# Optimization experiments

Hardware: AMD Instinct MI355X
Metric: run time of the kernel (lower is better)

The kernel has to match this reference:

```python
import jax, jax.numpy as jnp
import numpy as np

T, B, IN_DIM, MEM_DIM = 256, 64, 512, 512


def _kaiming(key, shape):
    # kaiming_normal_ default: fan_in = shape[1], gain = sqrt(2)
    std = np.sqrt(2.0 / shape[1])
    return jax.random.normal(key, shape, dtype=jnp.float32) * std


def setup_inputs() -> dict:
    key = jax.random.key(0)
    ks = jax.random.split(key, 10)
    inp = {
        "inputs": jax.random.normal(ks[0], (T, B, IN_DIM), dtype=jnp.float32),
        "emb_s": jax.random.normal(ks[1], (T, B, IN_DIM), dtype=jnp.float32),
        "c0": jnp.zeros((B, MEM_DIM), dtype=jnp.float32),
        "h0": jnp.zeros((B, MEM_DIM), dtype=jnp.float32),
        # learned params (torch Linear: y = x @ W.T + b)
        "W_ioux": _kaiming(ks[2], (4 * MEM_DIM, IN_DIM)),
        "b_ioux": jnp.zeros((4 * MEM_DIM,), jnp.float32),
        "W_iouh": _kaiming(ks[3], (4 * MEM_DIM, MEM_DIM)),
        "b_iouh": jnp.zeros((4 * MEM_DIM,), jnp.float32),
        "W_ious": _kaiming(ks[4], (4 * MEM_DIM, IN_DIM)),
        "b_ious": jnp.zeros((4 * MEM_DIM,), jnp.float32),
        "W_fx": _kaiming(ks[5], (MEM_DIM, IN_DIM)),
        "b_fx": jnp.zeros((MEM_DIM,), jnp.float32),
        "W_fh": _kaiming(ks[6], (MEM_DIM, MEM_DIM)),
        "b_fh": jnp.zeros((MEM_DIM,), jnp.float32),
        "W_wc": _kaiming(ks[7], (MEM_DIM, IN_DIM)),
        "b_wc": jnp.zeros((MEM_DIM,), jnp.float32),
    }
    return inp


def reference(inputs, emb_s, c0, h0,
              W_ioux, b_ioux, W_iouh, b_iouh, W_ious, b_ious,
              W_fx, b_fx, W_fh, b_fh, W_wc, b_wc):
    M = W_fh.shape[0]
    # Precompute all input-dependent projections for the whole sequence (big GEMMs).
    iou_x = (jnp.einsum('tbi,gi->tbg', inputs, W_ioux) + b_ioux
             + jnp.einsum('tbi,gi->tbg', emb_s, W_ious) + b_ious)      # [T,B,4M]
    ctelta_x = jnp.einsum('tbi,mi->tbm', inputs, W_fx) + b_fx          # [T,B,M]
    wc_s = jnp.tanh(jnp.einsum('tbi,mi->tbm', emb_s, W_wc) + b_wc)    # [T,B,M]

    def step(carry, xs):
        c, h = carry
        iou_t, ctx_t, wcs_t = xs
        iou = iou_t + h @ W_iouh.T + b_iouh                            # [B,4M]
        f, i, o, o_c = jnp.split(jax.nn.sigmoid(iou), 4, axis=1)
        c_telta = jnp.tanh(ctx_t + h @ W_fh.T + b_fh)
        c_new = i * c_telta + f * c
        h_new = o * jnp.tanh(c_new) + o_c * wcs_t
        return (c_new, h_new), h_new

    (c_fin, h_fin), out = jax.lax.scan(step, (c0, h0), (iou_x, ctelta_x, wc_s))
    return out, (c_fin, h_fin)
```

## Files before the change

kernel.cpp:

```cpp
#include <hip/hip_runtime.h>
#include <stdint.h>

#define T_STEPS 256
#define B_DIM   64
#define MDIM    512
#define NROWS   (T_STEPS * B_DIM)
#define KCAT    1024
#define NBIG    3072
#define W2ROWS  2560
#define NBLK2   32
#define OUT_N   ((size_t)T_STEPS * B_DIM * MDIM)

typedef short v8s __attribute__((ext_vector_type(8)));
typedef float v4f __attribute__((ext_vector_type(4)));

static __device__ __forceinline__ unsigned short f2bf(float f) {
    unsigned u = __builtin_bit_cast(unsigned, f);
    u += 0x7FFFu + ((u >> 16) & 1u);
    return (unsigned short)(u >> 16);
}
static __device__ __forceinline__ float bf2f(unsigned short h) {
    unsigned u = ((unsigned)h) << 16;
    return __builtin_bit_cast(float, u);
}
static __device__ __forceinline__ float sigmoidf(float x) {
    return 1.0f / (1.0f + __expf(-x));
}


__global__ void pack_xcat(const float* __restrict__ x, const float* __restrict__ s,
                          unsigned short* __restrict__ xcat) {
    int idx = blockIdx.x * blockDim.x + threadIdx.x;
    if (idx >= NROWS * KCAT) return;
    int row = idx >> 10, col = idx & 1023;
    float v = (col < 512) ? x[row * 512 + col] : s[row * 512 + (col - 512)];
    xcat[idx] = f2bf(v);
}

__global__ void pack_wbig(const float* __restrict__ Wioux, const float* __restrict__ bioux,
                          const float* __restrict__ Wious, const float* __restrict__ bious,
                          const float* __restrict__ Wfx,   const float* __restrict__ bfx,
                          const float* __restrict__ Wwc,   const float* __restrict__ bwc,
                          unsigned short* __restrict__ wbig, float* __restrict__ bbig) {
    int idx = blockIdx.x * blockDim.x + threadIdx.x;
    if (idx >= NBIG * KCAT) return;
    int r = idx >> 10, c = idx & 1023;
    float v;
    if (r < 2048)      v = (c < 512) ? Wioux[r * 512 + c] : Wious[r * 512 + (c - 512)];
    else if (r < 2560) { int j = r - 2048; v = (c < 512) ? Wfx[j * 512 + c] : 0.0f; }
    else               { int j = r - 2560; v = (c < 512) ? 0.0f : Wwc[j * 512 + (c - 512)]; }
    wbig[idx] = f2bf(v);
    if (c == 0) {
        float b;
        if (r < 2048)      b = bioux[r] + bious[r];
        else if (r < 2560) b = bfx[r - 2048];
        else               b = bwc[r - 2560];
        bbig[r] = b;
    }
}

__global__ void pack_w2(const float* __restrict__ Wiouh, const float* __restrict__ biouh,
                        const float* __restrict__ Wfh,   const float* __restrict__ bfh,
                        unsigned short* __restrict__ w2, float* __restrict__ b2) {
    int idx = blockIdx.x * blockDim.x + threadIdx.x;
    if (idx >= W2ROWS * 512) return;
    int r = idx >> 9, k = idx & 511;
    int bk = r / 80, rem = r % 80, g = rem >> 4, j = rem & 15;
    int m = bk * 16 + j;
    float v, bias;
    if (g < 4) { v = Wiouh[(size_t)(g * 512 + m) * 512 + k]; bias = biouh[g * 512 + m]; }
    else       { v = Wfh[(size_t)m * 512 + k];               bias = bfh[m]; }
    w2[idx] = f2bf(v);
    if (k == 0) b2[r] = bias;
}

__global__ void init_state(const float* __restrict__ h0,
                           unsigned short* __restrict__ hbuf0,
                           int* __restrict__ cnt) {
    int idx = blockIdx.x * blockDim.x + threadIdx.x;
    if (idx >= B_DIM * MDIM) return;
    hbuf0[idx] = f2bf(h0[idx]);
    if (idx == 0) *cnt = 0;
}


__global__ __launch_bounds__(256) void gemm_big(
        const unsigned short* __restrict__ xcat,
        const unsigned short* __restrict__ wbig,
        const float* __restrict__ bbig,
        unsigned short* __restrict__ yall) {
    __shared__ __align__(16) unsigned short As[128][40];
    __shared__ __align__(16) unsigned short Bs[128][40];
    int nb = blockIdx.x;
    int mb = blockIdx.y;
    int tid = threadIdx.x;
    int lane = tid & 63, wid = tid >> 6;
    int wm = wid & 1, wn = wid >> 1;
    int lm = lane & 15, lq = lane >> 4;
    v4f acc[4][4] = {};
    for (int kb = 0; kb < KCAT / 32; ++kb) {
        __syncthreads();
        #pragma unroll
        for (int it = 0; it < 2; ++it) {
            int cid = tid + it * 256;
            int r = cid >> 2, q = cid & 3;
            *(uint4*)&As[r][q * 8] =
                *(const uint4*)(xcat + (size_t)(mb * 128 + r) * KCAT + kb * 32 + q * 8);
            *(uint4*)&Bs[r][q * 8] =
                *(const uint4*)(wbig + (size_t)(nb * 128 + r) * KCAT + kb * 32 + q * 8);
        }
        __syncthreads();
        v8s a[4], b[4];
        #pragma unroll
        for (int i = 0; i < 4; ++i) a[i] = *(const v8s*)&As[wm * 64 + i * 16 + lm][lq * 8];
        #pragma unroll
        for (int j = 0; j < 4; ++j) b[j] = *(const v8s*)&Bs[wn * 64 + j * 16 + lm][lq * 8];
        #pragma unroll
        for (int i = 0; i < 4; ++i)
            #pragma unroll
            for (int j = 0; j < 4; ++j)
                acc[i][j] = __builtin_amdgcn_mfma_f32_16x16x32_bf16(a[i], b[j], acc[i][j], 0, 0, 0);
    }
    #pragma unroll
    for (int i = 0; i < 4; ++i) {
        int gm = mb * 128 + wm * 64 + i * 16 + lq * 4;
        #pragma unroll
        for (int j = 0; j < 4; ++j) {
            int gn = nb * 128 + wn * 64 + j * 16 + lm;
            float bias = bbig[gn];
            bool do_tanh = (gn >= 2560);
            #pragma unroll
            for (int r = 0; r < 4; ++r) {
                float v = acc[i][j][r] + bias;
                if (do_tanh) v = tanhf(v);
                yall[(size_t)(gm + r) * NBIG + gn] = f2bf(v);
            }
        }
    }
}


__device__ __forceinline__ void grid_barrier(int* cnt, int target) {
    __syncthreads();
    if (threadIdx.x == 0) {
        __hip_atomic_fetch_add(cnt, 1, __ATOMIC_ACQ_REL, __HIP_MEMORY_SCOPE_AGENT);
        while (__hip_atomic_load(cnt, __ATOMIC_ACQUIRE, __HIP_MEMORY_SCOPE_AGENT) < target)
            __builtin_amdgcn_s_sleep(1);
    }
    __syncthreads();
}

__global__ __launch_bounds__(256, 1) void lstm_persist(
        const unsigned short* __restrict__ yall,
        const unsigned short* __restrict__ w2,
        const float* __restrict__ b2,
        const float* __restrict__ c0,
        unsigned short* __restrict__ hbuf0,
        unsigned short* __restrict__ hbuf1,
        float* __restrict__ out,
        int* __restrict__ cnt) {
    __shared__ __align__(16) float red[2][10][256];
    __shared__ __align__(16) unsigned short ybuf[2][64][6][16];
    int bk = blockIdx.x;
    int tid = threadIdx.x;
    int lane = tid & 63, wid = tid >> 6;
    int p = wid >> 1;
    int q = wid & 1;
    int lm = lane & 15, lq = lane >> 4;
    int m = bk * 16 + lm;

    v8s bfrag[5][8];
    const unsigned short* w2b = w2 + (size_t)(bk * 80 + lm) * 512 + lq * 8;
    #pragma unroll
    for (int g = 0; g < 5; ++g)
        #pragma unroll
        for (int j = 0; j < 8; ++j)
            bfrag[g][j] = *(const v8s*)(w2b + (size_t)g * 16 * 512 + (q * 8 + j) * 32);

    float bias[5];
    #pragma unroll
    for (int g = 0; g < 5; ++g) bias[g] = b2[(bk * 5 + g) * 16 + lm];
    float creg[2][4];
    #pragma unroll
    for (int tb = 0; tb < 2; ++tb)
        #pragma unroll
        for (int r = 0; r < 4; ++r)
            creg[tb][r] = c0[(p * 32 + tb * 16 + lq * 4 + r) * 512 + m];

    if (q == 1) {
        #pragma unroll
        for (int i = 0; i < 6; ++i) {
            int c = (p * 6 + i) * 64 + lane;
            int b = c / 12, rem = c % 12, g = rem >> 1, half = rem & 1;
            int gcol = (g < 4) ? g * 512 : (g == 4 ? 2048 : 2560);
            const unsigned short* gp = yall + (size_t)b * NBIG + gcol + bk * 16 + half * 8;
            unsigned short* lp = &ybuf[0][0][0][0] + (p * 6 + i) * 512;
            __builtin_amdgcn_global_load_lds(
                (const __attribute__((address_space(1))) unsigned int*)gp,
                (__attribute__((address_space(3))) unsigned int*)lp, 16, 0, 0);
        }
    }

    for (int t = 0; t < T_STEPS; ++t) {
        const unsigned short* hin = (t & 1) ? hbuf1 : hbuf0;
        unsigned short*      hout = (t & 1) ? hbuf0 : hbuf1;
        v4f acc[2][5] = {};
        const unsigned short* ha = hin + (size_t)(p * 32 + lm) * 512 + q * 256 + lq * 8;
        #pragma unroll
        for (int j = 0; j < 8; ++j) {
            v8s a0 = *(const v8s*)(ha + j * 32);
            v8s a1 = *(const v8s*)(ha + 16 * 512 + j * 32);
            #pragma unroll
            for (int g = 0; g < 5; ++g) {
                acc[0][g] = __builtin_amdgcn_mfma_f32_16x16x32_bf16(a0, bfrag[g][j], acc[0][g], 0, 0, 0);
                acc[1][g] = __builtin_amdgcn_mfma_f32_16x16x32_bf16(a1, bfrag[g][j], acc[1][g], 0, 0, 0);
            }
        }
        if (q == 1) {
            #pragma unroll
            for (int tb = 0; tb < 2; ++tb)
                #pragma unroll
                for (int g = 0; g < 5; ++g)
                    *(v4f*)&red[p][tb * 5 + g][lane * 4] = acc[tb][g];
        }
        __syncthreads();
        if (q == 0) {
            #pragma unroll
            for (int tb = 0; tb < 2; ++tb)
                #pragma unroll
                for (int g = 0; g < 5; ++g)
                    acc[tb][g] += *(const v4f*)&red[p][tb * 5 + g][lane * 4];
            const unsigned short* yb = &ybuf[t & 1][0][0][0];
            #pragma unroll
            for (int tb = 0; tb < 2; ++tb) {
                #pragma unroll
                for (int r = 0; r < 4; ++r) {
                    int brow = p * 32 + tb * 16 + lq * 4 + r;
                    const unsigned short* ybr = yb + brow * 96;
                    float f_ = sigmoidf(bf2f(ybr[0 * 16 + lm]) + acc[tb][0][r] + bias[0]);
                    float i_ = sigmoidf(bf2f(ybr[1 * 16 + lm]) + acc[tb][1][r] + bias[1]);
                    float o_ = sigmoidf(bf2f(ybr[2 * 16 + lm]) + acc[tb][2][r] + bias[2]);
                    float oc = sigmoidf(bf2f(ybr[3 * 16 + lm]) + acc[tb][3][r] + bias[3]);
                    float ct = tanhf  (bf2f(ybr[4 * 16 + lm]) + acc[tb][4][r] + bias[4]);
                    float wcs = bf2f(ybr[5 * 16 + lm]);
                    float cn = i_ * ct + f_ * creg[tb][r];
                    creg[tb][r] = cn;
                    float hn = o_ * tanhf(cn) + oc * wcs;
                    out[((size_t)t * 64 + brow) * 512 + m] = hn;
                    hout[brow * 512 + m] = f2bf(hn);
                    if (t == T_STEPS - 1)
                        out[OUT_N + 32768 + (size_t)brow * 512 + m] = hn;
                }
            }
        } else if (t + 1 < T_STEPS) {
            int buf = (t + 1) & 1;
            #pragma unroll
            for (int i = 0; i < 6; ++i) {
                int c = (p * 6 + i) * 64 + lane;
                int b = c / 12, rem = c % 12, g = rem >> 1, half = rem & 1;
                int gcol = (g < 4) ? g * 512 : (g == 4 ? 2048 : 2560);
                const unsigned short* gp = yall + ((size_t)(t + 1) * 64 + b) * NBIG + gcol + bk * 16 + half * 8;
                unsigned short* lp = &ybuf[buf][0][0][0] + (p * 6 + i) * 512;
                __builtin_amdgcn_global_load_lds(
                    (const __attribute__((address_space(1))) unsigned int*)gp,
                    (__attribute__((address_space(3))) unsigned int*)lp, 16, 0, 0);
            }
        }
        grid_barrier(cnt, NBLK2 * (t + 1));
    }

    if (q == 0) {
        #pragma unroll
        for (int tb = 0; tb < 2; ++tb)
            #pragma unroll
            for (int r = 0; r < 4; ++r)
                out[OUT_N + (size_t)(p * 32 + tb * 16 + lq * 4 + r) * 512 + m] = creg[tb][r];
    }
}


extern "C" void kernel_launch(void* const* d_in, const int* in_sizes, int n_in,
                              void* d_out, int out_size, void* d_ws, size_t ws_size,
                              hipStream_t stream) {
    const float* inputs = (const float*)d_in[0];
    const float* emb_s  = (const float*)d_in[1];
    const float* c0     = (const float*)d_in[2];
    const float* h0     = (const float*)d_in[3];
    const float* W_ioux = (const float*)d_in[4];  const float* b_ioux = (const float*)d_in[5];
    const float* W_iouh = (const float*)d_in[6];  const float* b_iouh = (const float*)d_in[7];
    const float* W_ious = (const float*)d_in[8];  const float* b_ious = (const float*)d_in[9];
    const float* W_fx   = (const float*)d_in[10]; const float* b_fx   = (const float*)d_in[11];
    const float* W_fh   = (const float*)d_in[12]; const float* b_fh   = (const float*)d_in[13];
    const float* W_wc   = (const float*)d_in[14]; const float* b_wc   = (const float*)d_in[15];
    float* out = (float*)d_out;

    char* ws = (char*)d_ws;
    size_t off = 0;
    auto alloc = [&](size_t bytes) -> void* {
        void* p = ws + off;
        off += (bytes + 255) & ~(size_t)255;
        return p;
    };
    unsigned short* yall  = (unsigned short*)alloc((size_t)NROWS * NBIG * 2);
    unsigned short* xcat  = (unsigned short*)alloc((size_t)NROWS * KCAT * 2);
    unsigned short* wbig  = (unsigned short*)alloc((size_t)NBIG * KCAT * 2);
    float*          bbig  = (float*)alloc(NBIG * 4);
    unsigned short* w2    = (unsigned short*)alloc((size_t)W2ROWS * 512 * 2);
    float*          b2    = (float*)alloc(W2ROWS * 4);
    unsigned short* hbuf0 = (unsigned short*)alloc(B_DIM * MDIM * 2);
    unsigned short* hbuf1 = (unsigned short*)alloc(B_DIM * MDIM * 2);
    int*            cnt   = (int*)alloc(256);

    pack_xcat<<<(NROWS * KCAT + 255) / 256, 256, 0, stream>>>(inputs, emb_s, xcat);
    pack_wbig<<<(NBIG * KCAT + 255) / 256, 256, 0, stream>>>(
        W_ioux, b_ioux, W_ious, b_ious, W_fx, b_fx, W_wc, b_wc, wbig, bbig);
    pack_w2<<<(W2ROWS * 512 + 255) / 256, 256, 0, stream>>>(W_iouh, b_iouh, W_fh, b_fh, w2, b2);
    init_state<<<(B_DIM * MDIM + 255) / 256, 256, 0, stream>>>(h0, hbuf0, cnt);

    dim3 g1(NBIG / 128, NROWS / 128);
    gemm_big<<<g1, 256, 0, stream>>>(xcat, wbig, bbig, yall);

    lstm_persist<<<NBLK2, 256, 0, stream>>>(yall, w2, b2, c0, hbuf0, hbuf1, out, cnt);
}
```

Baseline: 2.320 ms.

## Replace atomic-counter grid barrier with per-block flag barrier and relaxed atomics

Replaces the single shared fetch-add counter grid barrier with per-block arrival flags on padded cache lines, which one wavefront polls in parallel with relaxed atomic loads instead of sleeping on one contended counter. Hidden-state stores and loads become relaxed agent-scope atomics so they bypass stale caches without acquire/release fences. The next step's yall prefetch moves to the top of the loop, and the post-reduction __syncthreads becomes a raw lgkmcnt wait plus s_barrier. This targets per-step barrier latency in the 256-step serial recurrence, at the cost of relying on vmcnt waits for memory ordering instead of formal acquire/release semantics.

Measured after the change: 2.666 ms. 14.9% more time.

```diff
diff --git a/kernel.cpp b/kernel.cpp
--- a/kernel.cpp
+++ b/kernel.cpp
@@ -25,6 +25,12 @@
 }
 static __device__ __forceinline__ float sigmoidf(float x) {
     return 1.0f / (1.0f + __expf(-x));
+}
+static __device__ __forceinline__ v8s load_h8(const unsigned short* p) {
+    ulonglong2 t;
+    t.x = __hip_atomic_load((const unsigned long long*)p,       __ATOMIC_RELAXED, __HIP_MEMORY_SCOPE_AGENT);
+    t.y = __hip_atomic_load((const unsigned long long*)(p + 4), __ATOMIC_RELAXED, __HIP_MEMORY_SCOPE_AGENT);
+    return __builtin_bit_cast(v8s, t);
 }
 
 
@@ -76,11 +82,12 @@
 
 __global__ void init_state(const float* __restrict__ h0,
                            unsigned short* __restrict__ hbuf0,
-                           int* __restrict__ cnt) {
+                           int* __restrict__ arrive) {
     int idx = blockIdx.x * blockDim.x + threadIdx.x;
     if (idx >= B_DIM * MDIM) return;
-    hbuf0[idx] = f2bf(h0[idx]);
-    if (idx == 0) *cnt = 0;
+    __hip_atomic_store(&hbuf0[idx], f2bf(h0[idx]), __ATOMIC_RELAXED, __HIP_MEMORY_SCOPE_AGENT);
+    if (idx < NBLK2)
+        __hip_atomic_store(&arrive[idx * 32], 0, __ATOMIC_RELAXED, __HIP_MEMORY_SCOPE_AGENT);
 }
 
 
@@ -140,16 +147,6 @@
 }
 
 
-__device__ __forceinline__ void grid_barrier(int* cnt, int target) {
-    __syncthreads();
-    if (threadIdx.x == 0) {
-        __hip_atomic_fetch_add(cnt, 1, __ATOMIC_ACQ_REL, __HIP_MEMORY_SCOPE_AGENT);
-        while (__hip_atomic_load(cnt, __ATOMIC_ACQUIRE, __HIP_MEMORY_SCOPE_AGENT) < target)
-            __builtin_amdgcn_s_sleep(1);
-    }
-    __syncthreads();
-}
-
 __global__ __launch_bounds__(256, 1) void lstm_persist(
         const unsigned short* __restrict__ yall,
         const unsigned short* __restrict__ w2,
@@ -158,7 +155,7 @@
         unsigned short* __restrict__ hbuf0,
         unsigned short* __restrict__ hbuf1,
         float* __restrict__ out,
-        int* __restrict__ cnt) {
+        int* __restrict__ arrive) {
     __shared__ __align__(16) float red[2][10][256];
     __shared__ __align__(16) unsigned short ybuf[2][64][6][16];
     int bk = blockIdx.x;
@@ -200,22 +197,43 @@
                 (__attribute__((address_space(3))) unsigned int*)lp, 16, 0, 0);
         }
     }
+    __syncthreads();
 
     for (int t = 0; t < T_STEPS; ++t) {
         const unsigned short* hin = (t & 1) ? hbuf1 : hbuf0;
         unsigned short*      hout = (t & 1) ? hbuf0 : hbuf1;
+
+        if (q == 1 && t + 1 < T_STEPS) {
+            int buf = (t + 1) & 1;
+            #pragma unroll
+            for (int i = 0; i < 6; ++i) {
+                int c = (p * 6 + i) * 64 + lane;
+                int b = c / 12, rem = c % 12, g = rem >> 1, half = rem & 1;
+                int gcol = (g < 4) ? g * 512 : (g == 4 ? 2048 : 2560);
+                const unsigned short* gp = yall + ((size_t)(t + 1) * 64 + b) * NBIG + gcol + bk * 16 + half * 8;
+                unsigned short* lp = &ybuf[buf][0][0][0] + (p * 6 + i) * 512;
+                __builtin_amdgcn_global_load_lds(
+                    (const __attribute__((address_space(1))) unsigned int*)gp,
+                    (__attribute__((address_space(3))) unsigned int*)lp, 16, 0, 0);
+            }
+        }
+
+        const unsigned short* ha = hin + (size_t)(p * 32 + lm) * 512 + q * 256 + lq * 8;
+        v8s af[2][8];
+        #pragma unroll
+        for (int j = 0; j < 8; ++j) {
+            af[0][j] = load_h8(ha + j * 32);
+            af[1][j] = load_h8(ha + 16 * 512 + j * 32);
+        }
         v4f acc[2][5] = {};
-        const unsigned short* ha = hin + (size_t)(p * 32 + lm) * 512 + q * 256 + lq * 8;
-        #pragma unroll
-        for (int j = 0; j < 8; ++j) {
-            v8s a0 = *(const v8s*)(ha + j * 32);
-            v8s a1 = *(const v8s*)(ha + 16 * 512 + j * 32);
+        #pragma unroll
+        for (int j = 0; j < 8; ++j)
             #pragma unroll
             for (int g = 0; g < 5; ++g) {
-                acc[0][g] = __builtin_amdgcn_mfma_f32_16x16x32_bf16(a0, bfrag[g][j], acc[0][g], 0, 0, 0);
-                acc[1][g] = __builtin_amdgcn_mfma_f32_16x16x32_bf16(a1, bfrag[g][j], acc[1][g], 0, 0, 0);
-            }
-        }
+                acc[0][g] = __builtin_amdgcn_mfma_f32_16x16x32_bf16(af[0][j], bfrag[g][j], acc[0][g], 0, 0, 0);
+                acc[1][g] = __builtin_amdgcn_mfma_f32_16x16x32_bf16(af[1][j], bfrag[g][j], acc[1][g], 0, 0, 0);
+            }
+
         if (q == 1) {
             #pragma unroll
             for (int tb = 0; tb < 2; ++tb)
@@ -223,7 +241,9 @@
                 for (int g = 0; g < 5; ++g)
                     *(v4f*)&red[p][tb * 5 + g][lane * 4] = acc[tb][g];
         }
-        __syncthreads();
+        asm volatile("s_waitcnt lgkmcnt(0)" ::: "memory");
+        __builtin_amdgcn_s_barrier();
+
         if (q == 0) {
             #pragma unroll
             for (int tb = 0; tb < 2; ++tb)
@@ -247,26 +267,31 @@
                     creg[tb][r] = cn;
                     float hn = o_ * tanhf(cn) + oc * wcs;
                     out[((size_t)t * 64 + brow) * 512 + m] = hn;
-                    hout[brow * 512 + m] = f2bf(hn);
+                    __hip_atomic_store(&hout[brow * 512 + m], f2bf(hn),
+                                       __ATOMIC_RELAXED, __HIP_MEMORY_SCOPE_AGENT);
                     if (t == T_STEPS - 1)
                         out[OUT_N + 32768 + (size_t)brow * 512 + m] = hn;
                 }
             }
-        } else if (t + 1 < T_STEPS) {
-            int buf = (t + 1) & 1;
-            #pragma unroll
-            for (int i = 0; i < 6; ++i) {
-                int c = (p * 6 + i) * 64 + lane;
-                int b = c / 12, rem = c % 12, g = rem >> 1, half = rem & 1;
-                int gcol = (g < 4) ? g * 512 : (g == 4 ? 2048 : 2560);
-                const unsigned short* gp = yall + ((size_t)(t + 1) * 64 + b) * NBIG + gcol + bk * 16 + half * 8;
-                unsigned short* lp = &ybuf[buf][0][0][0] + (p * 6 + i) * 512;
-                __builtin_amdgcn_global_load_lds(
-                    (const __attribute__((address_space(1))) unsigned int*)gp,
-                    (__attribute__((address_space(3))) unsigned int*)lp, 16, 0, 0);
-            }
-        }
-        grid_barrier(cnt, NBLK2 * (t + 1));
+        }
+
+        if (t + 1 < T_STEPS) {
+            asm volatile("s_waitcnt vmcnt(0)" ::: "memory");
+            __syncthreads();
+            if (wid == 0) {
+                if (lane == 0)
+                    __hip_atomic_store(&arrive[bk * 32], t + 1,
+                                       __ATOMIC_RELAXED, __HIP_MEMORY_SCOPE_AGENT);
+                if (lane < NBLK2) {
+                    int v;
+                    do {
+                        v = __hip_atomic_load(&arrive[lane * 32],
+                                              __ATOMIC_RELAXED, __HIP_MEMORY_SCOPE_AGENT);
+                    } while (v < t + 1);
+                }
+            }
+            __syncthreads();
+        }
     }
 
     if (q == 0) {
@@ -309,16 +334,16 @@
     float*          b2    = (float*)alloc(W2ROWS * 4);
     unsigned short* hbuf0 = (unsigned short*)alloc(B_DIM * MDIM * 2);
     unsigned short* hbuf1 = (unsigned short*)alloc(B_DIM * MDIM * 2);
-    int*            cnt   = (int*)alloc(256);
+    int*            arrive = (int*)alloc(NBLK2 * 32 * 4);
 
     pack_xcat<<<(NROWS * KCAT + 255) / 256, 256, 0, stream>>>(inputs, emb_s, xcat);
     pack_wbig<<<(NBIG * KCAT + 255) / 256, 256, 0, stream>>>(
         W_ioux, b_ioux, W_ious, b_ious, W_fx, b_fx, W_wc, b_wc, wbig, bbig);
     pack_w2<<<(W2ROWS * 512 + 255) / 256, 256, 0, stream>>>(W_iouh, b_iouh, W_fh, b_fh, w2, b2);
-    init_state<<<(B_DIM * MDIM + 255) / 256, 256, 0, stream>>>(h0, hbuf0, cnt);
+    init_state<<<(B_DIM * MDIM + 255) / 256, 256, 0, stream>>>(h0, hbuf0, arrive);
 
     dim3 g1(NBIG / 128, NROWS / 128);
     gemm_big<<<g1, 256, 0, stream>>>(xcat, wbig, bbig, yall);
 
-    lstm_persist<<<NBLK2, 256, 0, stream>>>(yall, w2, b2, c0, hbuf0, hbuf1, out, cnt);
-}
+    lstm_persist<<<NBLK2, 256, 0, stream>>>(yall, w2, b2, c0, hbuf0, hbuf1, out, arrive);
+}
```
